# Performance work log

Measured on AMD Instinct MI355X. Metric: run time of the kernel, lower is better.

## Reference

```python
import jax, jax.numpy as jnp
import numpy as np

NS, NP, EJ, ER = 10000, 2048, 32768, 32768  # skills, job/resume pairs, edges
D, H = 1536, 8
NEG_SLOPE_ATT = 0.2   # GAT attention leaky_relu
NEG_SLOPE = 0.01      # F.leaky_relu / nn.LeakyReLU default


def setup_inputs() -> dict:
    key = jax.random.key(0)
    ks = jax.random.split(key, 20)
    rn = lambda k, shp, s=1.0: jax.random.normal(k, shp, dtype=jnp.float32) * s
    s_d = 1.0 / np.sqrt(D)
    return {
        "x_skill": rn(ks[0], (NS, D)),
        "x_job": rn(ks[1], (NP, D)),
        "x_resume": rn(ks[2], (NP, D)),
        # GraphConv params (lin_rel has bias, lin_root bias=False in PyG)
        "W_rel": rn(ks[3], (D, D), s_d),
        "b_rel": jnp.zeros((D,), jnp.float32),
        "W_root": rn(ks[4], (D, D), s_d),
        # GATConv params (heads=8, concat=False)
        "W_gat_src": rn(ks[5], (D, H * D), s_d),
        "W_gat_dst": rn(ks[6], (D, H * D), s_d),
        "att_src": rn(ks[7], (H, D), s_d),
        "att_dst": rn(ks[8], (H, D), s_d),
        "b_gat": jnp.zeros((D,), jnp.float32),
        # MLP: [3072 -> 512 -> 128 -> 1]
        "W1": rn(ks[9], (2 * D, 512), 1.0 / np.sqrt(2 * D)),
        "b1": jnp.zeros((512,), jnp.float32),
        "W2": rn(ks[10], (512, 128), 1.0 / np.sqrt(512)),
        "b2": jnp.zeros((128,), jnp.float32),
        "W3": rn(ks[11], (128, 1), 1.0 / np.sqrt(128)),
        "b3": jnp.zeros((1,), jnp.float32),
        # edge lists (src = skill idx, dst = job/resume idx)
        "edge_src_job": jax.random.randint(ks[12], (EJ,), 0, NS, dtype=jnp.int32),
        "edge_dst_job": jax.random.randint(ks[13], (EJ,), 0, NP, dtype=jnp.int32),
        "edge_src_res": jax.random.randint(ks[14], (ER,), 0, NS, dtype=jnp.int32),
        "edge_dst_res": jax.random.randint(ks[15], (ER,), 0, NP, dtype=jnp.int32),
    }


def reference(x_skill, x_job, x_resume, W_rel, b_rel, W_root,
              W_gat_src, W_gat_dst, att_src, att_dst, b_gat,
              W1, b1, W2, b2, W3, b3,
              edge_src_job, edge_dst_job, edge_src_res, edge_dst_res):
    n_pair = x_job.shape[0]

    # --- GraphConv (skill -> job): sum-aggregate then linear + root ---
    agg = jax.ops.segment_sum(x_skill[edge_src_job], edge_dst_job,
                              num_segments=n_pair)                  # [NP, D]
    h_job = agg @ W_rel + b_rel + x_job @ W_root                     # [NP, D]

    # --- GATConv (skill -> resume), heads=H, concat=False, no self-loops ---
    xs = (x_skill @ W_gat_src).reshape(-1, H, D)                     # [NS, H, D]
    xd = (x_resume @ W_gat_dst).reshape(-1, H, D)                    # [NP, H, D]
    a_src = jnp.einsum('nhd,hd->nh', xs, att_src)                    # [NS, H]
    a_dst = jnp.einsum('nhd,hd->nh', xd, att_dst)                    # [NP, H]
    e = jax.nn.leaky_relu(a_src[edge_src_res] + a_dst[edge_dst_res],
                          NEG_SLOPE_ATT)                             # [E, H]
    # segment softmax over edges grouped by destination resume node
    e_max = jax.ops.segment_max(e, edge_dst_res, num_segments=n_pair)
    e_exp = jnp.exp(e - e_max[edge_dst_res])
    denom = jax.ops.segment_sum(e_exp, edge_dst_res, num_segments=n_pair)
    alpha = e_exp / (denom[edge_dst_res] + 1e-16)                    # [E, H]
    msg = xs[edge_src_res] * alpha[:, :, None]                       # [E, H, D]
    out = jax.ops.segment_sum(msg, edge_dst_res, num_segments=n_pair)  # [NP, H, D]
    h_res = out.mean(axis=1) + b_gat                                 # concat=False -> head mean

    # --- combine + MLP ---
    h = jnp.concatenate([jax.nn.leaky_relu(h_job, NEG_SLOPE),
                         jax.nn.leaky_relu(h_res, NEG_SLOPE)], axis=1)  # [NP, 2D]
    h = jax.nn.leaky_relu(h @ W1 + b1, NEG_SLOPE)
    h = jax.nn.leaky_relu(h @ W2 + b2, NEG_SLOPE)
    score = (h @ W3 + b3).squeeze(-1)                                # [NP]
    return score, alpha
```

## Files before the change

kernel.cpp:

```cpp
#include <hip/hip_runtime.h>

#define D_ 1536
#define H_ 8

typedef __attribute__((ext_vector_type(8))) short bf16x8;
typedef __attribute__((ext_vector_type(4))) float f32x4;

__device__ __forceinline__ unsigned short f2bf(float f) {
    unsigned u = __builtin_bit_cast(unsigned, f);
    unsigned r = (u + 0x7fffu + ((u >> 16) & 1u)) >> 16;
    return (unsigned short)r;
}

__device__ __forceinline__ unsigned pack2bf(float a, float b) {
    return (unsigned)f2bf(a) | ((unsigned)f2bf(b) << 16);
}

__device__ __forceinline__ float bflo(unsigned u) { return __builtin_bit_cast(float, u << 16); }
__device__ __forceinline__ float bfhi(unsigned u) { return __builtin_bit_cast(float, u & 0xffff0000u); }

__device__ __forceinline__ void gload16(const void* g, void* l) {
    __builtin_amdgcn_global_load_lds((const __attribute__((address_space(1))) void*)g,
                                     (__attribute__((address_space(3))) void*)l, 16, 0, 0);
}

__global__ __launch_bounds__(256) void k_prep(const float* __restrict__ W_gd,
                                              const float* __restrict__ att_d,
                                              float* __restrict__ Vdst,
                                              const float* __restrict__ W_gs,
                                              const float* __restrict__ att_s,
                                              float* __restrict__ Vsrc,
                                              unsigned short* __restrict__ BTg,
                                              const float* __restrict__ W_rel,
                                              const float* __restrict__ W_root,
                                              unsigned short* __restrict__ BT1,
                                              const float* __restrict__ W1,
                                              unsigned short* __restrict__ BTw1,
                                              const int* __restrict__ edj, int EJ,
                                              const int* __restrict__ edr, int ER,
                                              int* cnt_j, int* cnt_r) {
    __shared__ float t[64][65];
    __shared__ float red[4][H_];
    int r = blockIdx.x;

    if (r < D_) {
        int d = r;
        const float4* wr = (const float4*)(W_gd + (size_t)d * (H_ * D_));
        int tid = threadIdx.x;
        float part[H_];
        #pragma unroll
        for (int h = 0; h < H_; h++) {
            const float4* ar = (const float4*)(att_d + h * D_);
            float4 w0 = wr[h * 384 + tid];
            float4 a0 = ar[tid];
            float s = w0.x * a0.x + w0.y * a0.y + w0.z * a0.z + w0.w * a0.w;
            if (tid < 128) {
                float4 w1 = wr[h * 384 + 256 + tid];
                float4 a1 = ar[256 + tid];
                s += w1.x * a1.x + w1.y * a1.y + w1.z * a1.z + w1.w * a1.w;
            }
            part[h] = s;
        }
        int lane = tid & 63, w = tid >> 6;
        #pragma unroll
        for (int h = 0; h < H_; h++) {
            float v = part[h];
            for (int o = 32; o; o >>= 1) v += __shfl_down(v, o);
            if (lane == 0) red[w][h] = v;
        }
        __syncthreads();
        if (tid < H_) Vdst[d * H_ + tid] = red[0][tid] + red[1][tid] + red[2][tid] + red[3][tid];
        return;
    }
    r -= D_;

    if (r >= 6144) {
        int i = (r - 6144) * 256 + threadIdx.x;
        if (i < EJ) atomicAdd(&cnt_j[edj[i]], 1);
        else if (i < EJ + ER) atomicAdd(&cnt_r[edr[i - EJ]], 1);
        return;
    }

    const float* in; int ldin; unsigned short* out; int ldout; int nx; int gatb;
    if (r < 4608)               { in = W_gs;  ldin = 0;   out = BTg;      ldout = H_ * D_; nx = 24; gatb = 1; }
    else if ((r -= 4608) < 576) { in = W_rel; ldin = D_;  out = BT1;      ldout = 2 * D_;  nx = 24; gatb = 0; }
    else if ((r -= 576) < 576)  { in = W_root;ldin = D_;  out = BT1 + D_; ldout = 2 * D_;  nx = 24; gatb = 0; }
    else { r -= 576;              in = W1;    ldin = 512; out = BTw1;     ldout = 2 * D_;  nx = 8;  gatb = 0; }

    int n0 = (r % nx) * 64, k0 = (r / nx) * 64;
    int tx = threadIdx.x & 63, ty = threadIdx.x >> 6;
    #pragma unroll
    for (int i = 0; i < 16; i++) {
        int k = k0 + ty + i * 4;
        const float* rp;
        if (gatb) {
            int d2 = k % D_, h = k / D_;
            rp = in + (size_t)d2 * (H_ * D_) + (size_t)h * D_;
        } else {
            rp = in + (size_t)k * ldin;
        }
        t[ty + i * 4][tx] = rp[n0 + tx];
    }
    __syncthreads();
    int tx2 = threadIdx.x & 31, ty2 = threadIdx.x >> 5;
    #pragma unroll
    for (int i = 0; i < 8; i++) {
        int nl = ty2 + i * 8;
        unsigned v = pack2bf(t[tx2 * 2][nl], t[tx2 * 2 + 1][nl]);
        *(unsigned*)(out + (size_t)(n0 + nl) * ldout + k0 + tx2 * 2) = v;
    }
    if (gatb) {
        int h = k0 / D_, d2b = k0 - h * D_;
        int kl = threadIdx.x >> 2, q = threadIdx.x & 3;
        const float* ar = att_s + (size_t)h * D_ + n0 + q * 16;
        float s = 0.f;
        #pragma unroll
        for (int i = 0; i < 16; i++) s += t[kl][q * 16 + i] * ar[i];
        s += __shfl_xor(s, 1);
        s += __shfl_xor(s, 2);
        if (q == 0) atomicAdd(&Vsrc[(size_t)(d2b + kl) * H_ + h], s);
    }
}

__global__ __launch_bounds__(256) void k_a2(const float* __restrict__ xs,
                                            const float* __restrict__ xr,
                                            const float* __restrict__ Vs,
                                            const float* __restrict__ Vd,
                                            float* __restrict__ a_s,
                                            float* __restrict__ a_d,
                                            unsigned* __restrict__ xb, int NS, int NPn,
                                            const int* __restrict__ cnt_j, int* off_j,
                                            const int* __restrict__ cnt_r, int* off_r) {
    int n = blockIdx.x;
    if (n >= NS + NPn) {
        if (threadIdx.x >= 64) return;
        int which = n - NS - NPn;
        const int* cnt = which ? cnt_r : cnt_j;
        int* off = which ? off_r : off_j;
        int lane = threadIdx.x;
        int chunk = (NPn + 63) / 64;
        int base = lane * chunk;
        int sum = 0;
        for (int i = 0; i < chunk; i++) { int idx = base + i; if (idx < NPn) sum += cnt[idx]; }
        int incl = sum;
        for (int o = 1; o < 64; o <<= 1) { int t = __shfl_up(incl, o); if (lane >= o) incl += t; }
        int run = incl - sum;
        for (int i = 0; i < chunk; i++) { int idx = base + i; if (idx < NPn) { off[idx] = run; run += cnt[idx]; } }
        if (lane == 63) off[NPn] = run;
        return;
    }
    int skill = n < NS;
    int row = skill ? n : n - NS;
    const float2* xrow = (const float2*)(skill ? xs : xr) + (size_t)row * 768;
    const float* V = skill ? Vs : Vd;
    float* out = (skill ? a_s : a_d) + (size_t)row * H_;
    unsigned* ob = xb + (size_t)row * 768;
    float part[H_] = {};
    #pragma unroll
    for (int j = 0; j < 3; j++) {
        int e = threadIdx.x + j * 256;
        float2 v = xrow[e];
        if (skill) ob[e] = pack2bf(v.x, v.y);
        const float* vp = V + (size_t)(2 * e) * H_;
        #pragma unroll
        for (int h = 0; h < H_; h++) part[h] += v.x * vp[h] + v.y * vp[h + H_];
    }
    __shared__ float red[4][H_];
    int lane = threadIdx.x & 63, w = threadIdx.x >> 6;
    #pragma unroll
    for (int h = 0; h < H_; h++) {
        float v = part[h];
        for (int o = 32; o; o >>= 1) v += __shfl_down(v, o);
        if (lane == 0) red[w][h] = v;
    }
    __syncthreads();
    if (threadIdx.x < H_) out[threadIdx.x] =
        red[0][threadIdx.x] + red[1][threadIdx.x] + red[2][threadIdx.x] + red[3][threadIdx.x];
}

__global__ void k_scatter(const int* __restrict__ dj, const int* __restrict__ sj, int ej,
                          const int* __restrict__ dr, const int* __restrict__ sr, int er,
                          const int* __restrict__ off_j, int* fill_j, int* srcv_j,
                          const int* __restrict__ off_r, int* fill_r, int* sid_r, int* srcv_r) {
    int i = blockIdx.x * blockDim.x + threadIdx.x;
    if (i < ej) {
        int p = dj[i];
        int slot = atomicAdd(&fill_j[p], 1);
        srcv_j[off_j[p] + slot] = sj[i];
    } else if (i < ej + er) {
        int e = i - ej;
        int p = dr[e];
        int slot = atomicAdd(&fill_r[p], 1);
        int idx = off_r[p] + slot;
        sid_r[idx] = e;
        srcv_r[idx] = sr[e];
    }
}

__global__ void k_softmax(const float* __restrict__ a_src, const float* __restrict__ a_dst,
                          const int* __restrict__ srcv, const int* __restrict__ sid,
                          const int* __restrict__ cnt, const int* __restrict__ off,
                          float* __restrict__ alpha_out, float* __restrict__ alpha_s) {
    int p = blockIdx.x;
    int n = cnt[p], o = off[p];
    if (n == 0) return;
    int lane = threadIdx.x;
    float4 ad0 = *(const float4*)(a_dst + (size_t)p * H_);
    float4 ad1 = *(const float4*)(a_dst + (size_t)p * H_ + 4);
    float adv[8] = {ad0.x, ad0.y, ad0.z, ad0.w, ad1.x, ad1.y, ad1.z, ad1.w};
    if (n <= 64) {
        int e = 0;
        float v[8];
        if (lane < n) {
            e = sid[o + lane];
            int s = srcv[o + lane];
            float4 s0 = *(const float4*)(a_src + (size_t)s * H_);
            float4 s1 = *(const float4*)(a_src + (size_t)s * H_ + 4);
            float sv[8] = {s0.x, s0.y, s0.z, s0.w, s1.x, s1.y, s1.z, s1.w};
            #pragma unroll
            for (int h = 0; h < H_; h++) {
                float t = sv[h] + adv[h];
                v[h] = t >= 0.f ? t : 0.2f * t;
            }
        } else {
            #pragma unroll
            for (int h = 0; h < H_; h++) v[h] = -3.4e38f;
        }
        float ex[8];
        #pragma unroll
        for (int h = 0; h < H_; h++) {
            float m = v[h];
            for (int o2 = 32; o2; o2 >>= 1) m = fmaxf(m, __shfl_xor(m, o2));
            float ev = (lane < n) ? expf(v[h] - m) : 0.f;
            float s = ev;
            for (int o2 = 32; o2; o2 >>= 1) s += __shfl_xor(s, o2);
            ex[h] = ev / (s + 1e-16f);
        }
        if (lane < n) {
            *(float4*)(alpha_out + (size_t)e * H_) = make_float4(ex[0], ex[1], ex[2], ex[3]);
            *(float4*)(alpha_out + (size_t)e * H_ + 4) = make_float4(ex[4], ex[5], ex[6], ex[7]);
            *(float4*)(alpha_s + (size_t)(o + lane) * H_) = make_float4(ex[0], ex[1], ex[2], ex[3]);
            *(float4*)(alpha_s + (size_t)(o + lane) * H_ + 4) = make_float4(ex[4], ex[5], ex[6], ex[7]);
        }
    } else {
        #pragma unroll 1
        for (int h = 0; h < H_; h++) {
            float ad = adv[h];
            float m = -3.4e38f;
            for (int i = lane; i < n; i += 64) {
                float v = a_src[(size_t)srcv[o + i] * H_ + h] + ad;
                v = v >= 0.f ? v : 0.2f * v;
                m = fmaxf(m, v);
            }
            for (int o2 = 32; o2; o2 >>= 1) m = fmaxf(m, __shfl_xor(m, o2));
            float s = 0.f;
            for (int i = lane; i < n; i += 64) {
                float v = a_src[(size_t)srcv[o + i] * H_ + h] + ad;
                v = v >= 0.f ? v : 0.2f * v;
                s += expf(v - m);
            }
            for (int o2 = 32; o2; o2 >>= 1) s += __shfl_xor(s, o2);
            float inv = 1.f / (s + 1e-16f);
            for (int i = lane; i < n; i += 64) {
                float v = a_src[(size_t)srcv[o + i] * H_ + h] + ad;
                v = v >= 0.f ? v : 0.2f * v;
                float a = expf(v - m) * inv;
                alpha_out[(size_t)sid[o + i] * H_ + h] = a;
                alpha_s[(size_t)(o + i) * H_ + h] = a;
            }
        }
    }
}

__global__ __launch_bounds__(256) void k_aggs(const unsigned* __restrict__ xb,
                                              const int* __restrict__ srcv_j,
                                              const int* __restrict__ cnt_j, const int* __restrict__ off_j,
                                              const int* __restrict__ srcv_r,
                                              const int* __restrict__ cnt_r, const int* __restrict__ off_r,
                                              const float* __restrict__ alpha_s,
                                              const float* __restrict__ x_job,
                                              unsigned* __restrict__ cat_u,
                                              unsigned* __restrict__ aggatt_u) {
    int p = blockIdx.x;
    if (blockIdx.y < 3) {
        int col = blockIdx.y * 256 + threadIdx.x;
        int n = cnt_j[p], o = off_j[p];
        float2 acc = {0.f, 0.f};
        int i = 0;
        for (; i + 2 <= n; i += 2) {
            unsigned v0 = xb[(size_t)srcv_j[o + i] * 768 + col];
            unsigned v1 = xb[(size_t)srcv_j[o + i + 1] * 768 + col];
            acc.x += bflo(v0) + bflo(v1);
            acc.y += bfhi(v0) + bfhi(v1);
        }
        if (i < n) {
            unsigned v = xb[(size_t)srcv_j[o + i] * 768 + col];
            acc.x += bflo(v); acc.y += bfhi(v);
        }
        unsigned* orow = cat_u + (size_t)p * 1536;
        orow[col] = pack2bf(acc.x, acc.y);
        float2 vj = ((const float2*)x_job)[(size_t)p * 768 + col];
        orow[768 + col] = pack2bf(vj.x, vj.y);
    } else {
        int col = (blockIdx.y - 3) * 256 + threadIdx.x;
        int n = cnt_r[p], o = off_r[p];
        const float* as = alpha_s + (size_t)o * H_;
        float2 acc[H_] = {};
        int i = 0;
        for (; i + 2 <= n; i += 2) {
            unsigned v0 = xb[(size_t)srcv_r[o + i] * 768 + col];
            unsigned v1 = xb[(size_t)srcv_r[o + i + 1] * 768 + col];
            float l0 = bflo(v0), h0 = bfhi(v0), l1 = bflo(v1), h1 = bfhi(v1);
            const float* a0 = as + (size_t)i * H_;
            const float* a1 = a0 + H_;
            #pragma unroll
            for (int h = 0; h < H_; h++) {
                float w0 = a0[h], w1 = a1[h];
                acc[h].x += w0 * l0 + w1 * l1;
                acc[h].y += w0 * h0 + w1 * h1;
            }
        }
        if (i < n) {
            unsigned v0 = xb[(size_t)srcv_r[o + i] * 768 + col];
            float l0 = bflo(v0), h0 = bfhi(v0);
            const float* a0 = as + (size_t)i * H_;
            #pragma unroll
            for (int h = 0; h < H_; h++) { acc[h].x += a0[h] * l0; acc[h].y += a0[h] * h0; }
        }
        unsigned* orow = aggatt_u + (size_t)p * (H_ * 768);
        #pragma unroll
        for (int h = 0; h < H_; h++)
            orow[h * 768 + col] = pack2bf(acc[h].x, acc[h].y);
    }
}

__global__ __launch_bounds__(512, 4) void gemm_sk(const unsigned short* __restrict__ A, int lda,
                                                  const unsigned short* __restrict__ BT, int ldb,
                                                  float* __restrict__ P, int N, int bs, int extra) {
    __shared__ unsigned short As[3][256 * 32];
    __shared__ unsigned short Bs[3][128 * 32];
    int tid = threadIdx.x;
    int lane = tid & 63, wid = tid >> 6;

    int nwg = gridDim.x * gridDim.y;
    int bidh = blockIdx.y * gridDim.x + blockIdx.x;
    int swz = (bidh & 7) * (nwg >> 3) + (bidh >> 3);
    int bn = (swz % gridDim.x) * 128;
    int bm = (swz / gridDim.x) * 256;

    int z = blockIdx.z;
    int nt = bs + (z < extra);
    int kb = z * bs + min(z, extra);
    int kbase = kb * 32;

    int wr = wid >> 1, wc = wid & 1;
    int fr = lane & 15, g = lane >> 4;

    int ra0 = tid >> 2, sa0 = tid & 3;
    int ra1 = (tid + 512) >> 2;
    int sg_a0 = sa0 ^ ((ra0 >> 1) & 3);
    int sg_a1 = sa0 ^ ((ra1 >> 1) & 3);
    int sg_b = sg_a0;

    f32x4 acc[4][4] = {};

    auto stage = [&](int buf, int k0) {
        gload16(A + (size_t)(bm + ra0) * lda + k0 + sg_a0 * 8, &As[buf][tid * 8]);
        gload16(A + (size_t)(bm + ra1) * lda + k0 + sg_a1 * 8, &As[buf][(tid + 512) * 8]);
        gload16(BT + (size_t)(bn + ra0) * ldb + k0 + sg_b * 8, &Bs[buf][tid * 8]);
    };

    stage(0, kbase);
    if (nt > 1) stage(1, kbase + 32);
    for (int t = 0; t < nt; t++) {
        if (t + 2 < nt) {
            stage((t + 2) % 3, kbase + (t + 2) * 32);
            asm volatile("s_waitcnt vmcnt(6)" ::: "memory");
        } else if (t + 1 < nt) {
            asm volatile("s_waitcnt vmcnt(3)" ::: "memory");
        } else {
            asm volatile("s_waitcnt vmcnt(0)" ::: "memory");
        }
        __builtin_amdgcn_s_barrier();
        __builtin_amdgcn_sched_barrier(0);
        int cur = t % 3;
        bf16x8 a[4], b[4];
        #pragma unroll
        for (int mi = 0; mi < 4; mi++) {
            int row = wr * 64 + mi * 16 + fr;
            a[mi] = *(const bf16x8*)(&As[cur][row * 32 + ((g ^ ((row >> 1) & 3)) * 8)]);
        }
        #pragma unroll
        for (int ni = 0; ni < 4; ni++) {
            int row = wc * 64 + ni * 16 + fr;
            b[ni] = *(const bf16x8*)(&Bs[cur][row * 32 + ((g ^ ((row >> 1) & 3)) * 8)]);
        }
        __builtin_amdgcn_s_setprio(1);
        #pragma unroll
        for (int mi = 0; mi < 4; mi++)
            #pragma unroll
            for (int ni = 0; ni < 4; ni++)
                acc[mi][ni] = __builtin_amdgcn_mfma_f32_16x16x32_bf16(a[mi], b[ni], acc[mi][ni], 0, 0, 0);
        __builtin_amdgcn_s_setprio(0);
        __builtin_amdgcn_s_barrier();
        __builtin_amdgcn_sched_barrier(0);
    }

    size_t MN = (size_t)N * (size_t)(gridDim.y * 256);
    float* Pz = P + (size_t)z * MN;
    #pragma unroll
    for (int mi = 0; mi < 4; mi++) {
        int r0 = bm + wr * 64 + mi * 16 + (lane >> 4) * 4;
        #pragma unroll
        for (int ni = 0; ni < 4; ni++) {
            int c = bn + wc * 64 + ni * 16 + (lane & 15);
            #pragma unroll
            for (int j = 0; j < 4; j++)
                Pz[(size_t)(r0 + j) * N + c] = acc[mi][ni][j];
        }
    }
}

template <int OUT_BF16>
__global__ __launch_bounds__(256) void k_reduce(const float* __restrict__ P, int S, int MN, int N,
                                                void* __restrict__ Cout, int ldc,
                                                const float* __restrict__ bias, float scale,
                                                int useLeaky) {
    int idx = (blockIdx.x * 256 + threadIdx.x) * 4;
    if (idx >= MN) return;
    float4 v = *(const float4*)(P + idx);
    for (int s = 1; s < S; s++) {
        float4 t = *(const float4*)(P + (size_t)s * MN + idx);
        v.x += t.x; v.y += t.y; v.z += t.z; v.w += t.w;
    }
    int m = idx / N, n = idx - m * N;
    float vv[4] = {v.x, v.y, v.z, v.w};
    #pragma unroll
    for (int j = 0; j < 4; j++) {
        float x = vv[j] * scale + bias[n + j];
        if (useLeaky) x = x >= 0.f ? x : 0.01f * x;
        if (OUT_BF16) ((unsigned short*)Cout)[(size_t)m * ldc + n + j] = f2bf(x);
        else ((float*)Cout)[(size_t)m * ldc + n + j] = x;
    }
}

__global__ __launch_bounds__(256) void k_mlp2(const float* __restrict__ P, int MN1,
                                              const float* __restrict__ b1,
                                              const float* __restrict__ W2,
                                              const float* __restrict__ b2,
                                              const float* __restrict__ W3,
                                              const float* __restrict__ b3,
                                              float* __restrict__ score) {
    __shared__ unsigned h1s[8][256];
    __shared__ float red[4][4];
    int p0 = blockIdx.x * 8;
    int tid = threadIdx.x;
    #pragma unroll
    for (int i = 0; i < 8; i++) {
        int idx = tid + i * 256;
        int row = idx >> 8, c2 = idx & 255;
        size_t base = (size_t)(p0 + row) * 512 + 2 * c2;
        float2 v = {0.f, 0.f};
        #pragma unroll
        for (int s = 0; s < 8; s++) {
            float2 t = *(const float2*)(P + (size_t)s * MN1 + base);
            v.x += t.x; v.y += t.y;
        }
        float2 bb = *(const float2*)(b1 + 2 * c2);
        v.x += bb.x; v.y += bb.y;
        v.x = v.x >= 0.f ? v.x : 0.01f * v.x;
        v.y = v.y >= 0.f ? v.y : 0.01f * v.y;
        h1s[row][c2] = pack2bf(v.x, v.y);
    }
    __syncthreads();
    int c = tid & 127, rg = tid >> 7;
    float acc[4] = {};
    for (int k = 0; k < 512; k += 2) {
        float w0 = W2[(size_t)k * 128 + c];
        float w1 = W2[(size_t)(k + 1) * 128 + c];
        #pragma unroll
        for (int r = 0; r < 4; r++) {
            unsigned hv = h1s[rg * 4 + r][k >> 1];
            acc[r] += bflo(hv) * w0 + bfhi(hv) * w1;
        }
    }
    float w3 = W3[c];
    float pr[4];
    #pragma unroll
    for (int r = 0; r < 4; r++) {
        float v = acc[r] + b2[c];
        v = v >= 0.f ? v : 0.01f * v;
        pr[r] = v * w3;
    }
    #pragma unroll
    for (int r = 0; r < 4; r++)
        for (int o = 32; o; o >>= 1) pr[r] += __shfl_down(pr[r], o);
    int w = tid >> 6;
    if ((tid & 63) == 0) {
        #pragma unroll
        for (int r = 0; r < 4; r++) red[w][r] = pr[r];
    }
    __syncthreads();
    if (tid < 8) {
        int rg2 = tid >> 2, r = tid & 3;
        float s = red[rg2 * 2][r] + red[rg2 * 2 + 1][r] + b3[0];
        score[p0 + rg2 * 4 + r] = s;
    }
}

extern "C" void kernel_launch(void* const* d_in, const int* in_sizes, int n_in,
                              void* d_out, int out_size, void* d_ws, size_t ws_size,
                              hipStream_t stream) {
    const float* x_skill = (const float*)d_in[0];
    const float* x_job   = (const float*)d_in[1];
    const float* x_resume= (const float*)d_in[2];
    const float* W_rel   = (const float*)d_in[3];
    const float* b_rel   = (const float*)d_in[4];
    const float* W_root  = (const float*)d_in[5];
    const float* W_gs    = (const float*)d_in[6];
    const float* W_gd    = (const float*)d_in[7];
    const float* att_s   = (const float*)d_in[8];
    const float* att_d   = (const float*)d_in[9];
    const float* b_gat   = (const float*)d_in[10];
    const float* W1      = (const float*)d_in[11];
    const float* b1      = (const float*)d_in[12];
    const float* W2      = (const float*)d_in[13];
    const float* b2      = (const float*)d_in[14];
    const float* W3      = (const float*)d_in[15];
    const float* b3      = (const float*)d_in[16];
    const int* esj = (const int*)d_in[17];
    const int* edj = (const int*)d_in[18];
    const int* esr = (const int*)d_in[19];
    const int* edr = (const int*)d_in[20];

    const int NS = in_sizes[0] / D_;
    const int NP = in_sizes[1] / D_;
    const int EJ = in_sizes[17];
    const int ER = in_sizes[19];

    float* score = (float*)d_out;
    float* alpha = score + NP;

    char* ws = (char*)d_ws;
    size_t off = 0;
    auto alloc = [&](size_t bytes) -> void* {
        void* p = ws + off;
        off = (off + bytes + 255) & ~(size_t)255;
        return p;
    };

    int* cnt_j  = (int*)alloc((size_t)4 * NP * sizeof(int));
    int* fill_j = cnt_j + NP;
    int* cnt_r  = cnt_j + 2 * NP;
    int* fill_r = cnt_j + 3 * NP;
    int* off_j  = (int*)alloc((size_t)(NP + 1) * sizeof(int));
    int* off_r  = (int*)alloc((size_t)(NP + 1) * sizeof(int));
    int* srcv_j = (int*)alloc((size_t)EJ * sizeof(int));
    int* sid_r  = (int*)alloc((size_t)ER * sizeof(int));
    int* srcv_r = (int*)alloc((size_t)ER * sizeof(int));
    float* alpha_s = (float*)alloc((size_t)ER * H_ * sizeof(float));
    float* Vsrc = (float*)alloc((size_t)D_ * H_ * 4);
    float* Vdst = (float*)alloc((size_t)D_ * H_ * 4);
    float* a_src= (float*)alloc((size_t)NS * H_ * 4);
    float* a_dst= (float*)alloc((size_t)NP * H_ * 4);
    unsigned short* cat_in = (unsigned short*)alloc((size_t)NP * 2 * D_ * 2);
    unsigned short* aggatt = (unsigned short*)alloc((size_t)NP * H_ * D_ * 2);
    unsigned short* BT1    = (unsigned short*)alloc((size_t)D_ * 2 * D_ * 2);
    unsigned short* BTg    = (unsigned short*)alloc((size_t)D_ * H_ * D_ * 2);
    unsigned short* BTw1   = (unsigned short*)alloc((size_t)512 * 2 * D_ * 2);
    unsigned short* hcat   = (unsigned short*)alloc((size_t)NP * 2 * D_ * 2);
    float* Pbuf = (float*)alloc((size_t)5 * NP * D_ * 4);
    unsigned* xsb = (unsigned*)Pbuf;

    hipMemsetAsync(cnt_j, 0, (size_t)4 * NP * sizeof(int), stream);
    hipMemsetAsync(Vsrc, 0, (size_t)D_ * H_ * sizeof(float), stream);

    int egrid = (EJ + ER + 255) / 256;
    const int NPREP = D_ + 4608 + 576 + 576 + 384;

    k_prep<<<NPREP + egrid, 256, 0, stream>>>(
        W_gd, att_d, Vdst, W_gs, att_s, Vsrc, BTg, W_rel, W_root, BT1, W1, BTw1,
        edj, EJ, edr, ER, cnt_j, cnt_r);

    k_a2<<<NS + NP + 2, 256, 0, stream>>>(x_skill, x_resume, Vsrc, Vdst, a_src, a_dst, xsb,
                                          NS, NP, cnt_j, off_j, cnt_r, off_r);

    k_scatter<<<egrid, 256, 0, stream>>>(edj, esj, EJ, edr, esr, ER,
                                         off_j, fill_j, srcv_j,
                                         off_r, fill_r, sid_r, srcv_r);

    k_softmax<<<NP, 64, 0, stream>>>(a_src, a_dst, srcv_r, sid_r, cnt_r, off_r, alpha, alpha_s);
    k_aggs<<<dim3(NP, 6), 256, 0, stream>>>(xsb, srcv_j, cnt_j, off_j,
                                            srcv_r, cnt_r, off_r, alpha_s, x_job,
                                            (unsigned*)cat_in, (unsigned*)aggatt);

    const int MN_f = NP * D_;
    const int MN_1 = NP * 512;

    gemm_sk<<<dim3(D_ / 128, NP / 256, 5), 512, 0, stream>>>(
        cat_in, 2 * D_, BT1, 2 * D_, Pbuf, D_, 19, 1);
    k_reduce<1><<<MN_f / 1024, 256, 0, stream>>>(Pbuf, 5, MN_f, D_, hcat, 2 * D_, b_rel, 1.f, 1);

    gemm_sk<<<dim3(D_ / 128, NP / 256, 5), 512, 0, stream>>>(
        aggatt, H_ * D_, BTg, H_ * D_, Pbuf, D_, 76, 4);
    k_reduce<1><<<MN_f / 1024, 256, 0, stream>>>(Pbuf, 5, MN_f, D_, hcat + D_, 2 * D_, b_gat, 1.f / H_, 1);

    gemm_sk<<<dim3(512 / 128, NP / 256, 8), 512, 0, stream>>>(
        hcat, 2 * D_, BTw1, 2 * D_, Pbuf, 512, 12, 0);

    k_mlp2<<<NP / 8, 256, 0, stream>>>(Pbuf, MN_1, b1, W2, b2, W3, b3, score);
}
```

Before: 379.4 us.

## Merge GraphConv and GAT projection GEMMs into one launch with fused epilogue

Combines the GraphConv GEMM and the split-K GAT projection GEMM into a single kernel launch. Slice z=0 computes the full K=3072 GraphConv product without splitting and writes bias plus leaky_relu straight into hcat. Slices 1-5 produce the GAT split-K partials. This removes one launch and one reduce pass over a float partial buffer, and lets both GEMMs share the GPU. The risk is load imbalance: the z=0 slice runs 96 k-tiles against about 77 for the others, and its scalar bf16 stores are strided.

```diff
diff --git a/kernel.cpp b/kernel.cpp
--- a/kernel.cpp
+++ b/kernel.cpp
@@ -334,6 +334,122 @@
     }
 }
 
+__global__ __launch_bounds__(512, 4) void gemm_hcat(const unsigned short* __restrict__ Acat,
+                                                    const unsigned short* __restrict__ BT1,
+                                                    const unsigned short* __restrict__ Agat,
+                                                    const unsigned short* __restrict__ BTg,
+                                                    unsigned short* __restrict__ hcat,
+                                                    const float* __restrict__ b_rel,
+                                                    float* __restrict__ P) {
+    __shared__ unsigned short As[3][256 * 32];
+    __shared__ unsigned short Bs[3][128 * 32];
+    int tid = threadIdx.x;
+    int lane = tid & 63, wid = tid >> 6;
+
+    int nwg = gridDim.x * gridDim.y;
+    int bidh = blockIdx.y * gridDim.x + blockIdx.x;
+    int swz = (bidh & 7) * (nwg >> 3) + (bidh >> 3);
+    int bn = (swz % gridDim.x) * 128;
+    int bm = (swz / gridDim.x) * 256;
+
+    int z = blockIdx.z;
+    const unsigned short* A;
+    const unsigned short* BT;
+    int lda, kbase, nt;
+    if (z == 0) { A = Acat; BT = BT1; lda = 2 * D_; kbase = 0; nt = 96; }
+    else {
+        int zz = z - 1;
+        A = Agat; BT = BTg; lda = H_ * D_;
+        nt = 76 + (zz < 4);
+        kbase = (zz * 76 + min(zz, 4)) * 32;
+    }
+
+    int wr = wid >> 1, wc = wid & 1;
+    int fr = lane & 15, g = lane >> 4;
+
+    int ra0 = tid >> 2, sa0 = tid & 3;
+    int ra1 = (tid + 512) >> 2;
+    int sg_a0 = sa0 ^ ((ra0 >> 1) & 3);
+    int sg_a1 = sa0 ^ ((ra1 >> 1) & 3);
+    int sg_b = sg_a0;
+
+    f32x4 acc[4][4] = {};
+
+    auto stage = [&](int buf, int k0) {
+        gload16(A + (size_t)(bm + ra0) * lda + k0 + sg_a0 * 8, &As[buf][tid * 8]);
+        gload16(A + (size_t)(bm + ra1) * lda + k0 + sg_a1 * 8, &As[buf][(tid + 512) * 8]);
+        gload16(BT + (size_t)(bn + ra0) * lda + k0 + sg_b * 8, &Bs[buf][tid * 8]);
+    };
+
+    stage(0, kbase);
+    if (nt > 1) stage(1, kbase + 32);
+    for (int t = 0; t < nt; t++) {
+        if (t + 2 < nt) {
+            stage((t + 2) % 3, kbase + (t + 2) * 32);
+            asm volatile("s_waitcnt vmcnt(6)" ::: "memory");
+        } else if (t + 1 < nt) {
+            asm volatile("s_waitcnt vmcnt(3)" ::: "memory");
+        } else {
+            asm volatile("s_waitcnt vmcnt(0)" ::: "memory");
+        }
+        __builtin_amdgcn_s_barrier();
+        __builtin_amdgcn_sched_barrier(0);
+        int cur = t % 3;
+        bf16x8 a[4], b[4];
+        #pragma unroll
+        for (int mi = 0; mi < 4; mi++) {
+            int row = wr * 64 + mi * 16 + fr;
+            a[mi] = *(const bf16x8*)(&As[cur][row * 32 + ((g ^ ((row >> 1) & 3)) * 8)]);
+        }
+        #pragma unroll
+        for (int ni = 0; ni < 4; ni++) {
+            int row = wc * 64 + ni * 16 + fr;
+            b[ni] = *(const bf16x8*)(&Bs[cur][row * 32 + ((g ^ ((row >> 1) & 3)) * 8)]);
+        }
+        __builtin_amdgcn_s_setprio(1);
+        #pragma unroll
+        for (int mi = 0; mi < 4; mi++)
+            #pragma unroll
+            for (int ni = 0; ni < 4; ni++)
+                acc[mi][ni] = __builtin_amdgcn_mfma_f32_16x16x32_bf16(a[mi], b[ni], acc[mi][ni], 0, 0, 0);
+        __builtin_amdgcn_s_setprio(0);
+        __builtin_amdgcn_s_barrier();
+        __builtin_amdgcn_sched_barrier(0);
+    }
+
+    if (z == 0) {
+        #pragma unroll
+        for (int mi = 0; mi < 4; mi++) {
+            int r0 = bm + wr * 64 + mi * 16 + (lane >> 4) * 4;
+            #pragma unroll
+            for (int ni = 0; ni < 4; ni++) {
+                int c = bn + wc * 64 + ni * 16 + (lane & 15);
+                float bv = b_rel[c];
+                #pragma unroll
+                for (int j = 0; j < 4; j++) {
+                    float v = acc[mi][ni][j] + bv;
+                    v = v >= 0.f ? v : 0.01f * v;
+                    hcat[(size_t)(r0 + j) * (2 * D_) + c] = f2bf(v);
+                }
+            }
+        }
+    } else {
+        size_t MN = (size_t)D_ * (size_t)(gridDim.y * 256);
+        float* Pz = P + (size_t)(z - 1) * MN;
+        #pragma unroll
+        for (int mi = 0; mi < 4; mi++) {
+            int r0 = bm + wr * 64 + mi * 16 + (lane >> 4) * 4;
+            #pragma unroll
+            for (int ni = 0; ni < 4; ni++) {
+                int c = bn + wc * 64 + ni * 16 + (lane & 15);
+                #pragma unroll
+                for (int j = 0; j < 4; j++)
+                    Pz[(size_t)(r0 + j) * D_ + c] = acc[mi][ni][j];
+            }
+        }
+    }
+}
+
 __global__ __launch_bounds__(512, 4) void gemm_sk(const unsigned short* __restrict__ A, int lda,
                                                   const unsigned short* __restrict__ BT, int ldb,
                                                   float* __restrict__ P, int N, int bs, int extra) {
@@ -597,12 +713,8 @@
     const int MN_f = NP * D_;
     const int MN_1 = NP * 512;
 
-    gemm_sk<<<dim3(D_ / 128, NP / 256, 5), 512, 0, stream>>>(
-        cat_in, 2 * D_, BT1, 2 * D_, Pbuf, D_, 19, 1);
-    k_reduce<1><<<MN_f / 1024, 256, 0, stream>>>(Pbuf, 5, MN_f, D_, hcat, 2 * D_, b_rel, 1.f, 1);
-
-    gemm_sk<<<dim3(D_ / 128, NP / 256, 5), 512, 0, stream>>>(
-        aggatt, H_ * D_, BTg, H_ * D_, Pbuf, D_, 76, 4);
+    gemm_hcat<<<dim3(D_ / 128, NP / 256, 6), 512, 0, stream>>>(
+        cat_in, BT1, aggatt, BTg, hcat, b_rel, Pbuf);
     k_reduce<1><<<MN_f / 1024, 256, 0, stream>>>(Pbuf, 5, MN_f, D_, hcat + D_, 2 * D_, b_gat, 1.f / H_, 1);
 
     gemm_sk<<<dim3(512 / 128, NP / 256, 8), 512, 0, stream>>>(
```

Measured after the change: 390.9 us. 3.0% more time.
